# Optimization experiments

Hardware: AMD Instinct MI355X
Metric: run time of the kernel (lower is better)

The kernel has to match this reference:

```python
import math
import jax, jax.numpy as jnp
import numpy as np
from jax import lax

W_DIM = 512
UP = 2
K = 3
LRELU_GAIN = math.sqrt(2.0)  # bias_act def_gain for 'lrelu'
CLAMP = 256.0                # conv_clamp * gain(=1)


def setup_inputs() -> dict:
    key = jax.random.key(0)
    ks = jax.random.split(key, 8)
    B, Cin, Cout, H = 16, 512, 512, 32
    return {
        "x": jax.random.normal(ks[0], (B, Cin, H, H), jnp.float32),
        "w_latent": jax.random.normal(ks[1], (B, W_DIM), jnp.float32),
        "affine_weight": jax.random.normal(ks[2], (Cin, W_DIM), jnp.float32),
        "affine_bias": jnp.ones((Cin,), jnp.float32),  # bias_init=1
        "conv_weight": jax.random.normal(ks[3], (Cout, Cin, K, K), jnp.float32),
        "noise": jax.random.normal(ks[4], (B, 1, 2 * H, 2 * H), jnp.float32),
        "noise_strength": jax.random.uniform(ks[5], (1,), jnp.float32),
        "bias": jax.random.normal(ks[6], (Cout,), jnp.float32),
    }


def reference(x, w_latent, affine_weight, affine_bias, conv_weight, noise, noise_strength, bias):
    B, Cin, H, W = x.shape
    Cout = conv_weight.shape[0]

    # EqualFullyConnectedLayer (linear act): style = w @ (W * 1/sqrt(in)).T + b
    style = w_latent @ (affine_weight * (1.0 / math.sqrt(W_DIM))).T + affine_bias  # [B, Cin]

    # Modulate + demodulate per-sample weights: [B, Cout, Cin, K, K]
    wmod = conv_weight[None] * style[:, None, :, None, None]
    dcoefs = lax.rsqrt(jnp.sum(wmod * wmod, axis=(2, 3, 4)) + 1e-8)  # [B, Cout]
    wmod = wmod * dcoefs[:, :, None, None, None]

    # Grouped transposed conv (stride=UP), batch-as-groups trick.
    # torch.conv_transpose2d(x, w.transpose, stride=UP) == dilated conv with
    # spatially-flipped modulated weight, lhs_dilation=UP, padding=K-1.
    w_eff = wmod.reshape(B * Cout, Cin, K, K)[:, :, ::-1, ::-1]
    x1 = x.reshape(1, B * Cin, H, W)
    y = lax.conv_general_dilated(
        x1, w_eff, window_strides=(1, 1),
        padding=[(K - 1, K - 1), (K - 1, K - 1)],
        lhs_dilation=(UP, UP), feature_group_count=B,
        dimension_numbers=("NCHW", "OIHW", "NCHW"))  # [1, B*Cout, 2H+1, 2W+1]

    # upfirdn2d: FIR low-pass (1,3,3,1) outer, normalized, gain=up^2, pad (1,1,1,1)
    f1 = jnp.array([1.0, 3.0, 3.0, 1.0], jnp.float32)
    f2 = jnp.outer(f1, f1)
    f2 = f2 / f2.sum() * (UP * UP)
    yc = y.reshape(B * Cout, 1, 2 * H + 1, 2 * W + 1)
    y = lax.conv_general_dilated(
        yc, f2[None, None], window_strides=(1, 1), padding=[(1, 1), (1, 1)],
        dimension_numbers=("NCHW", "OIHW", "NCHW"))
    y = y.reshape(B, Cout, 2 * H, 2 * W)

    # noise injection + fused bias + lrelu(gain=sqrt(2)) + clamp
    y = y + noise * noise_strength[0]
    y = y + bias[None, :, None, None]
    y = jax.nn.leaky_relu(y, negative_slope=0.2) * LRELU_GAIN
    return jnp.clip(y, -CLAMP, CLAMP)
```

## Files before the change

### kernel.cpp

```cpp
#include <hip/hip_runtime.h>
#include <hip/hip_bf16.h>


typedef unsigned short u16;
typedef unsigned int u32;
typedef u16 u16x8 __attribute__((ext_vector_type(8)));
typedef __bf16 bf16x8 __attribute__((ext_vector_type(8)));
typedef float f32x4 __attribute__((ext_vector_type(4)));

#define NB 16

__device__ __forceinline__ float bf2f(u16 v) {
  unsigned int u = ((unsigned int)v) << 16;
  float f;
  __builtin_memcpy(&f, &u, 4);
  return f;
}
__device__ __forceinline__ u16 f2bf(float f) {
  __hip_bfloat16 h = __float2bfloat16(f);
  u16 r;
  __builtin_memcpy(&r, &h, 2);
  return r;
}
__device__ __forceinline__ void async16(u16* lds, const u16* g) {
  __builtin_amdgcn_global_load_lds(
      (const __attribute__((address_space(1))) u32*)g,
      (__attribute__((address_space(3))) u32*)lds, 16, 0, 0);
}

__global__ __launch_bounds__(256) void k_style(const float* __restrict__ wl,
                                               const float* __restrict__ aw,
                                               const float* __restrict__ ab,
                                               float* __restrict__ style) {
  __shared__ float lw[512];
  const int b = blockIdx.y;
  const int c = blockIdx.x * 256 + threadIdx.x;
  for (int k = threadIdx.x; k < 512; k += 256) lw[k] = wl[b * 512 + k];
  __syncthreads();
  const float* row = aw + (size_t)c * 512;
  float acc = 0.f;
#pragma unroll 8
  for (int k = 0; k < 512; ++k) acc += lw[k] * row[k];
  style[b * 512 + c] = acc * 0.04419417382415922f + ab[c];
}

__global__ __launch_bounds__(256) void k_dcoef(const float* __restrict__ cw,
                                               const float* __restrict__ style,
                                               float* __restrict__ dcoef) {
  __shared__ float wsq[512];
  const int o = blockIdx.x, t = threadIdx.x;
  for (int c = t; c < 512; c += 256) {
    const float* p = cw + (size_t)o * 4608 + (size_t)c * 9;
    float s = 0.f;
#pragma unroll
    for (int k = 0; k < 9; ++k) {
      float v = p[k];
      s += v * v;
    }
    wsq[c] = s;
  }
  __syncthreads();
  const int w = t >> 6, l = t & 63;
  for (int b = w; b < NB; b += 4) {
    float part = 0.f;
#pragma unroll
    for (int c = l; c < 512; c += 64) {
      float st = style[b * 512 + c];
      part += st * st * wsq[c];
    }
#pragma unroll
    for (int off = 32; off; off >>= 1) part += __shfl_down(part, off, 64);
    if (l == 0) dcoef[b * 512 + o] = 1.0f / sqrtf(part + 1e-8f);
  }
}

__global__ __launch_bounds__(256) void k_pack(const float* __restrict__ cw,
                                              u16* __restrict__ W2) {
  __shared__ u16 lw[4608];
  const int o = blockIdx.x, t = threadIdx.x;
  const float* src = cw + (size_t)o * 4608;
  for (int v = t; v < 4608; v += 256) {
    unsigned c = (unsigned)v / 9u;
    unsigned kp = (unsigned)v % 9u;
    lw[kp * 512 + c] = f2bf(src[v]);
  }
  __syncthreads();
  u16* dst = W2 + (size_t)o * 4608;
  for (int v = t; v < 576; v += 256)
    *(u16x8*)(dst + v * 8) = *(const u16x8*)(lw + v * 8);
}

__global__ __launch_bounds__(256) void k_xt(const float* __restrict__ x,
                                            const float* __restrict__ style,
                                            u16* __restrict__ xT) {
  __shared__ u16 tile[64 * 66];
  const int b = blockIdx.z, c0 = blockIdx.y << 6, s0 = blockIdx.x << 6;
  const int t = threadIdx.x;
#pragma unroll
  for (int i = 0; i < 16; ++i) {
    int e = i * 256 + t;
    int cc = e >> 6, ss = e & 63;
    int c = c0 + cc;
    float v = x[(size_t)(b * 512 + c) * 1024 + s0 + ss] * style[b * 512 + c];
    tile[cc * 66 + ss] = f2bf(v);
  }
  __syncthreads();
#pragma unroll
  for (int i = 0; i < 16; ++i) {
    int e = i * 256 + t;
    int sc = e >> 6, cx = e & 63;
    xT[(size_t)(b * 1024 + s0 + sc) * 512 + c0 + cx] = tile[cx * 66 + sc];
  }
}

__global__ __launch_bounds__(256) void k_gemm(const u16* __restrict__ W2,
                                              const u16* __restrict__ xT,
                                              u16* __restrict__ Z) {
  __shared__ u16 At[128 * 32];
  __shared__ u16 Bt[128 * 32];
  const int t = threadIdx.x;
  const int m0 = blockIdx.y << 7;
  const int n0 = blockIdx.x << 7;
  const int l = t & 63;
  const int w = t >> 6;
  const int wy = ((t >> 7) & 1) << 6;
  const int wx = ((t >> 6) & 1) << 6;
  const int lrow = l & 15;
  const int lk8 = (l >> 4) << 3;

  const u16* gA = W2 + (size_t)(m0 + (t >> 2)) * 512 + ((t & 3) << 3);
  const u16* gB = xT + (size_t)(n0 + (t >> 2)) * 512 + ((t & 3) << 3);
  u16* lA0 = At + (w << 9);
  u16* lA1 = At + 2048 + (w << 9);
  u16* lB0 = Bt + (w << 9);
  u16* lB1 = Bt + 2048 + (w << 9);

  f32x4 acc[4][4] = {};

  for (int k0 = 0; k0 < 512; k0 += 32) {
    async16(lA0, gA + k0);
    async16(lA1, gA + k0 + 64 * 512);
    async16(lB0, gB + k0);
    async16(lB1, gB + k0 + 64 * 512);
    asm volatile("s_waitcnt vmcnt(0)" ::: "memory");
    __syncthreads();
    bf16x8 av[4], bv[4];
#pragma unroll
    for (int i = 0; i < 4; ++i)
      av[i] = *(const bf16x8*)(At + (wy + i * 16 + lrow) * 32 + lk8);
#pragma unroll
    for (int j = 0; j < 4; ++j)
      bv[j] = *(const bf16x8*)(Bt + (wx + j * 16 + lrow) * 32 + lk8);
#pragma unroll
    for (int i = 0; i < 4; ++i)
#pragma unroll
      for (int j = 0; j < 4; ++j)
        acc[i][j] = __builtin_amdgcn_mfma_f32_16x16x32_bf16(av[i], bv[j], acc[i][j], 0, 0, 0);
    __syncthreads();
  }

  const int mr = m0 + wy + ((l >> 4) << 2);
  const int nc = n0 + wx + lrow;
#pragma unroll
  for (int i = 0; i < 4; ++i)
#pragma unroll
    for (int j = 0; j < 4; ++j)
#pragma unroll
      for (int r = 0; r < 4; ++r)
        Z[(size_t)(mr + i * 16 + r) * 16384 + nc + j * 16] = f2bf(acc[i][j][r]);
}

__global__ __launch_bounds__(256) void k_scatter(
    const u16* __restrict__ Z, const float* __restrict__ dcoef,
    const float* __restrict__ noise, const float* __restrict__ nstr,
    const float* __restrict__ bias, float* __restrict__ out) {
  __shared__ u16 Zl[9 * 1024];
  __shared__ float ybuf[67 * 68];
  const int o = blockIdx.x;
  const int b = blockIdx.y;
  const int t = threadIdx.x;
  const u16* Zp = Z + (size_t)o * 9 * 16384 + (size_t)b * 1024;
  for (int v = t; v < 1152; v += 256) {
    int kp = v >> 7, off = (v & 127) << 3;
    *(u16x8*)(Zl + kp * 1024 + off) = *(const u16x8*)(Zp + (size_t)kp * 16384 + off);
  }
  for (int i = t; i < 67 * 68; i += 256) ybuf[i] = 0.f;
  __syncthreads();
  for (int idx = t; idx < 65 * 65; idx += 256) {
    int p = idx / 65;
    int q = idx - p * 65;
    int ph = p >> 1, qh = q >> 1;
    int ky0 = p & 1;
    int kx0 = q & 1;
    bool vy0 = ph < 32;
    bool vy1 = !(p & 1) && (ph >= 1);
    bool vx0 = qh < 32;
    bool vx1 = !(q & 1) && (qh >= 1);
    float s = 0.f;
    if (vy0 && vx0) s += bf2f(Zl[(ky0 * 3 + kx0) * 1024 + ph * 32 + qh]);
    if (vy0 && vx1) s += bf2f(Zl[(ky0 * 3 + 2) * 1024 + ph * 32 + qh - 1]);
    if (vy1 && vx0) s += bf2f(Zl[(6 + kx0) * 1024 + (ph - 1) * 32 + qh]);
    if (vy1 && vx1) s += bf2f(Zl[8 * 1024 + (ph - 1) * 32 + qh - 1]);
    ybuf[(p + 1) * 68 + q + 1] = s;
  }
  __syncthreads();
  const float dc = dcoef[b * 512 + o];
  const float ns = nstr[0];
  const float bo = bias[o];
#pragma unroll
  for (int r = 0; r < 16; ++r) {
    int idx = r * 256 + t;
    int m = idx >> 6, n = idx & 63;
    float acc = 0.f;
#pragma unroll
    for (int u = 0; u < 4; ++u) {
      const float* row = ybuf + (m + u) * 68 + n;
      float rs = row[0] + 3.f * row[1] + 3.f * row[2] + row[3];
      acc += (u == 1 || u == 2) ? 3.f * rs : rs;
    }
    acc *= 0.0625f;
    float v = acc * dc + noise[(b << 12) + idx] * ns + bo;
    v = (v > 0.f ? v : 0.2f * v) * 1.4142135623730951f;
    v = fminf(fmaxf(v, -256.f), 256.f);
    out[((size_t)(b * 512 + o) << 12) + idx] = v;
  }
}

extern "C" void kernel_launch(void* const* d_in, const int* in_sizes, int n_in,
                              void* d_out, int out_size, void* d_ws, size_t ws_size,
                              hipStream_t stream) {
  const float* x = (const float*)d_in[0];
  const float* wl = (const float*)d_in[1];
  const float* aw = (const float*)d_in[2];
  const float* ab = (const float*)d_in[3];
  const float* cw = (const float*)d_in[4];
  const float* noise = (const float*)d_in[5];
  const float* nstr = (const float*)d_in[6];
  const float* bias = (const float*)d_in[7];
  float* out = (float*)d_out;

  float* style = (float*)d_ws;
  float* dcoef = style + 8192;
  u16* W2 = (u16*)(dcoef + 8192);
  u16* xT = W2 + 4608 * 512;
  u16* Z = xT + (size_t)16384 * 512;

  k_style<<<dim3(2, 16), 256, 0, stream>>>(wl, aw, ab, style);
  k_dcoef<<<dim3(512), 256, 0, stream>>>(cw, style, dcoef);
  k_pack<<<dim3(512), 256, 0, stream>>>(cw, W2);
  k_xt<<<dim3(16, 8, 16), 256, 0, stream>>>(x, style, xT);
  k_gemm<<<dim3(128, 36), 256, 0, stream>>>(W2, xT, Z);
  k_scatter<<<dim3(512, 16), 256, 0, stream>>>(Z, dcoef, noise, nstr, bias, out);
}
```

Measured before the change: 393.4 us.

## Fold transposed-conv scatter and FIR into separable polyphase passes

Replaces the scatter epilogue's two-stage approach (building a padded 65x65 intermediate in shared memory, then applying a 4x4 FIR stencil per output) with a polyphase decomposition. A horizontal pass combines the kernel-tap planes into per-row even/odd column values for each vertical tap. A vertical pass then produces two output rows per iteration from register-rotated values. This cuts shared-memory traffic, removes the zero-fill and the integer division, and lowers per-output arithmetic, at the cost of more intricate index logic and boundary handling.

```diff
diff --git a/kernel.cpp b/kernel.cpp
--- a/kernel.cpp
+++ b/kernel.cpp
@@ -175,7 +175,7 @@
     const float* __restrict__ noise, const float* __restrict__ nstr,
     const float* __restrict__ bias, float* __restrict__ out) {
   __shared__ u16 Zl[9 * 1024];
-  __shared__ float ybuf[67 * 68];
+  __shared__ float Hl[3 * 2048];
   const int o = blockIdx.x;
   const int b = blockIdx.y;
   const int t = threadIdx.x;
@@ -184,45 +184,62 @@
     int kp = v >> 7, off = (v & 127) << 3;
     *(u16x8*)(Zl + kp * 1024 + off) = *(const u16x8*)(Zp + (size_t)kp * 16384 + off);
   }
-  for (int i = t; i < 67 * 68; i += 256) ybuf[i] = 0.f;
-  __syncthreads();
-  for (int idx = t; idx < 65 * 65; idx += 256) {
-    int p = idx / 65;
-    int q = idx - p * 65;
-    int ph = p >> 1, qh = q >> 1;
-    int ky0 = p & 1;
-    int kx0 = q & 1;
-    bool vy0 = ph < 32;
-    bool vy1 = !(p & 1) && (ph >= 1);
-    bool vx0 = qh < 32;
-    bool vx1 = !(q & 1) && (qh >= 1);
-    float s = 0.f;
-    if (vy0 && vx0) s += bf2f(Zl[(ky0 * 3 + kx0) * 1024 + ph * 32 + qh]);
-    if (vy0 && vx1) s += bf2f(Zl[(ky0 * 3 + 2) * 1024 + ph * 32 + qh - 1]);
-    if (vy1 && vx0) s += bf2f(Zl[(6 + kx0) * 1024 + (ph - 1) * 32 + qh]);
-    if (vy1 && vx1) s += bf2f(Zl[8 * 1024 + (ph - 1) * 32 + qh - 1]);
-    ybuf[(p + 1) * 68 + q + 1] = s;
-  }
-  __syncthreads();
-  const float dc = dcoef[b * 512 + o];
+  __syncthreads();
+#pragma unroll
+  for (int e = 0; e < 12; ++e) {
+    int idx = e * 256 + t;
+    int ky = idx >> 10;
+    int i = (idx >> 5) & 31;
+    int j = idx & 31;
+    const u16* P0 = Zl + (ky * 3 + 0) * 1024 + i * 32;
+    const u16* P1 = P0 + 1024;
+    const u16* P2 = P0 + 2048;
+    float Ej = bf2f(P0[j]) + (j >= 1 ? bf2f(P2[j - 1]) : 0.f);
+    float Ej1 = (j < 31 ? bf2f(P0[j + 1]) : 0.f) + bf2f(P2[j]);
+    float Ojm = j >= 1 ? bf2f(P1[j - 1]) : 0.f;
+    float Oj = bf2f(P1[j]);
+    float Ojp = j < 31 ? bf2f(P1[j + 1]) : 0.f;
+    float* hp = Hl + ky * 2048 + i * 64 + j;
+    hp[0] = Ojm + 3.f * Ej + 3.f * Oj + Ej1;
+    hp[32] = Ej + 3.f * Oj + 3.f * Ej1 + Ojp;
+  }
+  __syncthreads();
+  const float dc = dcoef[b * 512 + o] * 0.0625f;
   const float ns = nstr[0];
   const float bo = bias[o];
-#pragma unroll
-  for (int r = 0; r < 16; ++r) {
-    int idx = r * 256 + t;
-    int m = idx >> 6, n = idx & 63;
-    float acc = 0.f;
-#pragma unroll
-    for (int u = 0; u < 4; ++u) {
-      const float* row = ybuf + (m + u) * 68 + n;
-      float rs = row[0] + 3.f * row[1] + 3.f * row[2] + row[3];
-      acc += (u == 1 || u == 2) ? 3.f * rs : rs;
-    }
-    acc *= 0.0625f;
-    float v = acc * dc + noise[(b << 12) + idx] * ns + bo;
-    v = (v > 0.f ? v : 0.2f * v) * 1.4142135623730951f;
-    v = fminf(fmaxf(v, -256.f), 256.f);
-    out[((size_t)(b * 512 + o) << 12) + idx] = v;
+  const int n = t & 63;
+  const int i0 = (t >> 6) << 3;
+  const int sw = ((n & 1) << 5) | (n >> 1);
+  const float* H0 = Hl + sw;
+  const float* H1 = Hl + 2048 + sw;
+  const float* H2 = Hl + 4096 + sw;
+  float h0 = H0[i0 * 64];
+  float h1 = H1[i0 * 64];
+  float h1p = (i0 > 0) ? H1[(i0 - 1) * 64] : 0.f;
+  float h2p = (i0 > 0) ? H2[(i0 - 1) * 64] : 0.f;
+  const float* nz = noise + ((size_t)b << 12) + n;
+  float* op = out + (((size_t)(b * 512 + o)) << 12) + n;
+#pragma unroll
+  for (int s = 0; s < 8; ++s) {
+    int i = i0 + s;
+    float h0n = (i < 31) ? H0[(i + 1) * 64] : 0.f;
+    float h1n = (i < 31) ? H1[(i + 1) * 64] : 0.f;
+    float h2 = H2[i * 64];
+    float ev = h1p + 3.f * (h0 + h2p) + 3.f * h1 + (h0n + h2);
+    float od = (h0 + h2p) + 3.f * h1 + 3.f * (h0n + h2) + h1n;
+    int m = 2 * i;
+    float v0 = ev * dc + nz[(size_t)m * 64] * ns + bo;
+    v0 = (v0 > 0.f ? v0 : 0.2f * v0) * 1.4142135623730951f;
+    v0 = fminf(fmaxf(v0, -256.f), 256.f);
+    op[(size_t)m * 64] = v0;
+    float v1 = od * dc + nz[(size_t)(m + 1) * 64] * ns + bo;
+    v1 = (v1 > 0.f ? v1 : 0.2f * v1) * 1.4142135623730951f;
+    v1 = fminf(fmaxf(v1, -256.f), 256.f);
+    op[(size_t)(m + 1) * 64] = v1;
+    h0 = h0n;
+    h1p = h1;
+    h1 = h1n;
+    h2p = h2;
   }
 }
 
```

After: 383.6 us. 1.03x faster.
